# Optimization experiments

Measured on AMD Instinct MI355X. Metric: run time of the kernel, lower is better.

Reference implementation:

```python
import jax, jax.numpy as jnp
import numpy as np

DT = 0.1
TAU_HP = 12.3  # Tm1 high-pass time constant
TAU_LP = 2.3   # Tm1 low-pass time constant

N_NEURONS = 200_000
N_EDGES = 6_400_000
N_TM1 = 25_000
STEPS = 50


def setup_inputs() -> dict:
    key = jax.random.key(0)
    k1, k2, k3, k4 = jax.random.split(key, 4)
    tm1_input = jax.random.normal(k1, (STEPS, N_TM1), dtype=jnp.float32)
    weights = jax.random.normal(k2, (N_EDGES,), dtype=jnp.float32) * 0.1
    tau = jnp.ones((N_NEURONS,), dtype=jnp.float32)      # tau_init = 1.0 per type
    vrest = jnp.zeros((N_NEURONS,), dtype=jnp.float32)   # vrest_init = 0.0 per type
    source_idx = jax.random.randint(k3, (N_EDGES,), 0, N_NEURONS, dtype=jnp.int32)
    target_idx = jax.random.randint(k4, (N_EDGES,), 0, N_NEURONS, dtype=jnp.int32)
    return {
        "tm1_input": tm1_input,
        "weights": weights,
        "tau": tau,
        "vrest": vrest,
        "source_idx": source_idx,
        "target_idx": target_idx,
        "n_tm1": N_TM1,
    }


def reference(tm1_input, weights, tau, vrest, source_idx, target_idx, n_tm1):
    n_neurons = tau.shape[0]

    def step(carry, x):
        v, tm1_f, tm1_v = carry
        # Tm1 temporal filters: high-pass then rectify then low-pass
        hp_out = x - tm1_f                                   # [n_tm1]
        tm1_f_new = tm1_f + DT * (x - tm1_f) / TAU_HP
        rect_out = jax.nn.relu(hp_out)
        # write (old) tm1_v into the Tm1 slice of v before recurrence
        v = v.at[:n_tm1].set(tm1_v)
        tm1_v_new = tm1_v + DT * (rect_out - tm1_v) / TAU_LP
        # gather -> weight -> scatter-add message passing
        r = jax.nn.relu(v)                                   # [n_neurons]
        edge_currents = r[source_idx] * weights              # [n_edges]
        synaptic_input = jax.ops.segment_sum(
            edge_currents, target_idx, num_segments=n_neurons)
        external = jnp.zeros_like(v).at[:n_tm1].set(tm1_v_new)
        dv = (-v + synaptic_input + vrest + external) / tau
        dv = dv.at[:n_tm1].set(0.0)                          # Tm1 driven by its filters
        v = v + DT * dv
        return (v, tm1_f_new, tm1_v_new), None

    v0 = jnp.zeros((tau.shape[0],), dtype=tm1_input.dtype)
    f0 = jnp.zeros((n_tm1,), dtype=tm1_input.dtype)
    tv0 = jnp.zeros((n_tm1,), dtype=tm1_input.dtype)
    (v, _, _), _ = jax.lax.scan(step, (v0, f0, tv0), tm1_input)
    return v[None, :]  # [1, n_neurons], matches torch batch=1
```

## Files before the change

### kernel.cpp

```cpp
#include <hip/hip_runtime.h>
#include <hip/hip_bf16.h>

#define DT 0.1f
#define TAU_HP 12.3f
#define TAU_LP 2.3f
#define SCAN_B 1024

#define BSHIFT 7
#define BMASK 127
#define BMAX 2048
#define CHUNK 32768
#define B4_CAP 6144


__global__ void init_kernel(float* __restrict__ vA,
                            float* __restrict__ tm1_f,
                            int n_neurons, int n_tm1) {
    int i = blockIdx.x * blockDim.x + threadIdx.x;
    if (i < n_neurons) vA[i] = 0.0f;
    if (i < n_tm1) tm1_f[i] = 0.0f;
}

__global__ void bhist_kernel(const int* __restrict__ tgt, int* __restrict__ blkhist,
                             int n_edges, int n_tm1, int nb, int nblk) {
    __shared__ int hist[BMAX];
    int b = blockIdx.x;
    for (int i = threadIdx.x; i < nb; i += blockDim.x) hist[i] = 0;
    __syncthreads();
    int base = b * CHUNK;
    int end = min(base + CHUNK, n_edges);
    for (int k = base + threadIdx.x; k < end; k += blockDim.x) {
        int t = tgt[k];
        if (t >= n_tm1) atomicAdd(&hist[t >> BSHIFT], 1);
    }
    __syncthreads();
    for (int i = threadIdx.x; i < nb; i += blockDim.x)
        blkhist[(size_t)i * nblk + b] = hist[i];
}

__global__ void scan1_kernel(const int* in, int* out, int* bsums, int n) {
    __shared__ int s[SCAN_B];
    int gid = blockIdx.x * SCAN_B + threadIdx.x;
    int x = (gid < n) ? in[gid] : 0;
    s[threadIdx.x] = x;
    __syncthreads();
    for (int off = 1; off < SCAN_B; off <<= 1) {
        int t = (threadIdx.x >= off) ? s[threadIdx.x - off] : 0;
        __syncthreads();
        s[threadIdx.x] += t;
        __syncthreads();
    }
    if (gid < n) out[gid] = s[threadIdx.x] - x;
    if (threadIdx.x == SCAN_B - 1) bsums[blockIdx.x] = s[SCAN_B - 1];
}

__global__ void scan2_kernel(int* bsums, int nb, int* total) {
    __shared__ int s[SCAN_B];
    int x = (threadIdx.x < nb) ? bsums[threadIdx.x] : 0;
    s[threadIdx.x] = x;
    __syncthreads();
    for (int off = 1; off < SCAN_B; off <<= 1) {
        int t = (threadIdx.x >= off) ? s[threadIdx.x - off] : 0;
        __syncthreads();
        s[threadIdx.x] += t;
        __syncthreads();
    }
    if (threadIdx.x == nb - 1) *total = s[threadIdx.x];
    if (threadIdx.x < nb) bsums[threadIdx.x] = s[threadIdx.x] - x;
}

__global__ void scanadd_kernel(int* data, const int* __restrict__ bsums, int n) {
    int gid = blockIdx.x * blockDim.x + threadIdx.x;
    if (gid < n) data[gid] += bsums[gid / SCAN_B];
}

__global__ void bin_kernel(const int* __restrict__ src, const int* __restrict__ tgt,
                           const float* __restrict__ w, const int* __restrict__ scanned,
                           int2* __restrict__ edges, int n_edges, int n_tm1,
                           int nb, int nblk) {
    __shared__ int cur[BMAX];
    int b = blockIdx.x;
    for (int i = threadIdx.x; i < nb; i += blockDim.x)
        cur[i] = scanned[(size_t)i * nblk + b];
    __syncthreads();
    int base = b * CHUNK;
    int end = min(base + CHUNK, n_edges);
    for (int k = base + threadIdx.x; k < end; k += blockDim.x) {
        int t = tgt[k];
        if (t < n_tm1) continue;
        int pos = atomicAdd(&cur[t >> BSHIFT], 1);
        edges[pos] = make_int2(src[k] | ((t & BMASK) << 18), __float_as_int(w[k]));
    }
}

__global__ void finalize_kernel(int2* edges, const int* __restrict__ scanned,
                                int* __restrict__ row_start,
                                const int* __restrict__ total,
                                int n_neurons, int nb, int nblk) {
    __shared__ int2 buf[B4_CAP];
    __shared__ int hist[BMASK + 1], ls[BMASK + 1], cur[BMASK + 1];
    int b = blockIdx.x;
    int n_kept = *total;
    int beg = scanned[(size_t)b * nblk];
    int end = (b == nb - 1) ? n_kept : scanned[(size_t)(b + 1) * nblk];
    int n = min(end - beg, B4_CAP);

    for (int k = threadIdx.x; k < n; k += blockDim.x) buf[k] = edges[beg + k];
    if (threadIdx.x <= BMASK) hist[threadIdx.x] = 0;
    __syncthreads();
    for (int k = threadIdx.x; k < n; k += blockDim.x)
        atomicAdd(&hist[(buf[k].x >> 18) & BMASK], 1);
    __syncthreads();
    if (threadIdx.x <= BMASK) ls[threadIdx.x] = hist[threadIdx.x];
    __syncthreads();
    for (int off = 1; off <= BMASK; off <<= 1) {
        int t = (threadIdx.x <= BMASK && threadIdx.x >= off) ? ls[threadIdx.x - off] : 0;
        __syncthreads();
        if (threadIdx.x <= BMASK) ls[threadIdx.x] += t;
        __syncthreads();
    }
    if (threadIdx.x <= BMASK) {
        int excl = ls[threadIdx.x] - hist[threadIdx.x];
        cur[threadIdx.x] = excl;
        int t = (b << BSHIFT) + threadIdx.x;
        if (t < n_neurons) row_start[t] = beg + excl;
    }
    if (b == nb - 1 && threadIdx.x == 0) row_start[n_neurons] = n_kept;
    __syncthreads();
    for (int k = threadIdx.x; k < n; k += blockDim.x) {
        int2 r = buf[k];
        int pos = atomicAdd(&cur[(r.x >> 18) & BMASK], 1);
        edges[beg + pos] = make_int2(r.x & 0x3FFFF, r.y);
    }
}

__global__ void step_kernel(const int* __restrict__ row_start,
                            const int2* __restrict__ edges,
                            const float* __restrict__ vr,
                            float* __restrict__ vw,
                            float* __restrict__ tm1_f,
                            const float* __restrict__ x,
                            const float* __restrict__ tau,
                            const float* __restrict__ vrest,
                            int n_neurons, int n_tm1, int gbase, int last) {
    int g = blockIdx.x * blockDim.x + threadIdx.x;

    if (g < n_tm1) {
        float cur = vr[g];
        if (last) {
            vw[g] = cur;
        } else {
            float f  = tm1_f[g];
            float xk = x[g];
            float hp = xk - f;
            tm1_f[g] = f + DT * (xk - f) / TAU_HP;
            vw[g] = cur + DT * (fmaxf(hp, 0.0f) - cur) / TAU_LP;
        }
        return;
    }
    if (g < gbase) return;

    int t = g - gbase;
    int row = n_tm1 + (t >> 3);
    if (row >= n_neurons) return;
    int lane = t & 7;

    int s = row_start[row];
    int e = row_start[row + 1];
    float sum = 0.0f;
    for (int p = (s & ~1) + 2 * lane; p < e; p += 16) {
        int4 q = *(const int4*)(edges + p);
        if (p >= s)    sum += fmaxf(vr[q.x], 0.0f) * __int_as_float(q.y);
        if (p + 1 < e) sum += fmaxf(vr[q.z], 0.0f) * __int_as_float(q.w);
    }
    sum += __shfl_xor(sum, 4);
    sum += __shfl_xor(sum, 2);
    sum += __shfl_xor(sum, 1);
    if (lane == 0) {
        float vi = vr[row];
        vw[row] = vi + DT * ((-vi + sum + vrest[row]) / tau[row]);
    }
}

extern "C" void kernel_launch(void* const* d_in, const int* in_sizes, int n_in,
                              void* d_out, int out_size, void* d_ws, size_t ws_size,
                              hipStream_t stream) {
    const float* tm1_input  = (const float*)d_in[0];
    const float* weights    = (const float*)d_in[1];
    const float* tau        = (const float*)d_in[2];
    const float* vrest      = (const float*)d_in[3];
    const int*   source_idx = (const int*)d_in[4];
    const int*   target_idx = (const int*)d_in[5];

    const int n_edges   = in_sizes[1];
    const int n_neurons = in_sizes[2];
    const int n_tm1     = 25000;
    const int steps     = in_sizes[0] / n_tm1;

    const int nb   = (n_neurons + BMASK) >> BSHIFT;
    const int nblk = (n_edges + CHUNK - 1) / CHUNK;
    const int n_scan = nb * nblk;

    size_t off = 0;
    auto alloc = [&](size_t n) { size_t o = off; off += n; return o; };
    int* ws_i = (int*)d_ws;
    float* ws_f = (float*)d_ws;

    int2*  edges     = (int2*)(ws_i + alloc((size_t)(n_edges + 2) * 2));
    float* vA        = ws_f + alloc(n_neurons);
    float* vB        = ws_f + alloc(n_neurons);
    float* tm1_f     = ws_f + alloc(n_tm1);
    int*   row_start = ws_i + alloc(n_neurons + 1);
    int*   blkhist   = ws_i + alloc((size_t)n_scan);
    int*   bsums     = ws_i + alloc(SCAN_B);
    int*   total     = ws_i + alloc(1);
    (void)ws_size;

    float* out = (float*)d_out;

    const int B = 256;
    const int gridN = (n_neurons + B - 1) / B;
    const int nScanBlocks = (n_scan + SCAN_B - 1) / SCAN_B;
    const int gridSA = (n_scan + B - 1) / B;

    const int gbase = (n_tm1 + 63) & ~63;
    const int work  = gbase + (n_neurons - n_tm1) * 8;
    const int gridG = (work + B - 1) / B;

    init_kernel<<<gridN, B, 0, stream>>>(vA, tm1_f, n_neurons, n_tm1);
    bhist_kernel<<<nblk, 1024, 0, stream>>>(target_idx, blkhist, n_edges, n_tm1,
                                            nb, nblk);
    scan1_kernel<<<nScanBlocks, SCAN_B, 0, stream>>>(blkhist, blkhist, bsums, n_scan);
    scan2_kernel<<<1, SCAN_B, 0, stream>>>(bsums, nScanBlocks, total);
    scanadd_kernel<<<gridSA, B, 0, stream>>>(blkhist, bsums, n_scan);
    bin_kernel<<<nblk, 1024, 0, stream>>>(source_idx, target_idx, weights, blkhist,
                                          edges, n_edges, n_tm1, nb, nblk);
    finalize_kernel<<<nb, 1024, 0, stream>>>(edges, blkhist, row_start, total,
                                             n_neurons, nb, nblk);

    for (int k = 0; k < steps; ++k) {
        const float* vr = (k & 1) ? vB : vA;
        float* vw = (k == steps - 1) ? out : ((k & 1) ? vA : vB);
        step_kernel<<<gridG, B, 0, stream>>>(
            row_start, edges, vr, vw, tm1_f,
            tm1_input + (size_t)k * n_tm1,
            tau, vrest, n_neurons, n_tm1, gbase, (k == steps - 1) ? 1 : 0);
    }
}
```

Baseline: 1.876 ms.

## Skip gathers from non-positive neurons using a per-step positivity bitmask

Each step now writes a bitmask marking which neurons ended with positive voltage, built with wave ballots and atomicOr. The next step's edge loop checks this compact bitmask before loading the source voltage, so it skips the scattered gather for neurons whose ReLU output is zero. Three mask buffers rotate so one can be cleared while another is read and a third is written. The cost is an extra bitmask load per edge, atomics per wave, and divergent branches in the gather loop. The benefit depends on how sparse the activity is, and early steps, where most voltages are zero, gain the most.

Measured after the change: 2.180 ms. 1.16x slower.

```diff
diff --git a/kernel.cpp b/kernel.cpp
--- a/kernel.cpp
+++ b/kernel.cpp
@@ -15,10 +15,12 @@
 
 __global__ void init_kernel(float* __restrict__ vA,
                             float* __restrict__ tm1_f,
-                            int n_neurons, int n_tm1) {
+                            unsigned* __restrict__ mask3,
+                            int n_neurons, int n_tm1, int mask3_words) {
     int i = blockIdx.x * blockDim.x + threadIdx.x;
     if (i < n_neurons) vA[i] = 0.0f;
     if (i < n_tm1) tm1_f[i] = 0.0f;
+    if (i < mask3_words) mask3[i] = 0u;
 }
 
 __global__ void bhist_kernel(const int* __restrict__ tgt, int* __restrict__ blkhist,
@@ -142,43 +144,75 @@
                             const float* __restrict__ x,
                             const float* __restrict__ tau,
                             const float* __restrict__ vrest,
+                            const unsigned* __restrict__ maskR,
+                            unsigned* __restrict__ maskW,
+                            unsigned* __restrict__ maskC,
+                            int mask_words,
                             int n_neurons, int n_tm1, int gbase, int last) {
     int g = blockIdx.x * blockDim.x + threadIdx.x;
 
-    if (g < n_tm1) {
-        float cur = vr[g];
-        if (last) {
-            vw[g] = cur;
-        } else {
-            float f  = tm1_f[g];
-            float xk = x[g];
-            float hp = xk - f;
-            tm1_f[g] = f + DT * (xk - f) / TAU_HP;
-            vw[g] = cur + DT * (fmaxf(hp, 0.0f) - cur) / TAU_LP;
+    if (g < gbase) {
+        if (g < mask_words) maskC[g] = 0u;
+        float val = 0.0f;
+        bool wrote = false;
+        if (g < n_tm1) {
+            float cur = vr[g];
+            if (last) {
+                val = cur;
+            } else {
+                float f  = tm1_f[g];
+                float xk = x[g];
+                float hp = xk - f;
+                tm1_f[g] = f + DT * (xk - f) / TAU_HP;
+                val = cur + DT * (fmaxf(hp, 0.0f) - cur) / TAU_LP;
+            }
+            vw[g] = val;
+            wrote = true;
         }
+        unsigned long long bm = __ballot(wrote && (val > 0.0f));
+        int l = threadIdx.x & 63;
+        unsigned lo = (unsigned)(bm & 0xffffffffull);
+        unsigned hi = (unsigned)(bm >> 32);
+        if (l == 0 && lo)  atomicOr(&maskW[g >> 5], lo);
+        if (l == 32 && hi) atomicOr(&maskW[g >> 5], hi);
         return;
     }
-    if (g < gbase) return;
 
     int t = g - gbase;
     int row = n_tm1 + (t >> 3);
-    if (row >= n_neurons) return;
     int lane = t & 7;
-
-    int s = row_start[row];
-    int e = row_start[row + 1];
+    bool active = (row < n_neurons);
     float sum = 0.0f;
-    for (int p = (s & ~1) + 2 * lane; p < e; p += 16) {
-        int4 q = *(const int4*)(edges + p);
-        if (p >= s)    sum += fmaxf(vr[q.x], 0.0f) * __int_as_float(q.y);
-        if (p + 1 < e) sum += fmaxf(vr[q.z], 0.0f) * __int_as_float(q.w);
+    float vnew = 0.0f;
+
+    if (active) {
+        int s = row_start[row];
+        int e = row_start[row + 1];
+        for (int p = (s & ~1) + 2 * lane; p < e; p += 16) {
+            int4 q = *(const int4*)(edges + p);
+            if (p >= s && ((maskR[q.x >> 5] >> (q.x & 31)) & 1u))
+                sum += vr[q.x] * __int_as_float(q.y);
+            if (p + 1 < e && ((maskR[q.z >> 5] >> (q.z & 31)) & 1u))
+                sum += vr[q.z] * __int_as_float(q.w);
+        }
     }
     sum += __shfl_xor(sum, 4);
     sum += __shfl_xor(sum, 2);
     sum += __shfl_xor(sum, 1);
-    if (lane == 0) {
+    if (active && lane == 0) {
         float vi = vr[row];
-        vw[row] = vi + DT * ((-vi + sum + vrest[row]) / tau[row]);
+        vnew = vi + DT * ((-vi + sum + vrest[row]) / tau[row]);
+        vw[row] = vnew;
+    }
+    unsigned long long bm = __ballot(active && lane == 0 && vnew > 0.0f);
+    if ((threadIdx.x & 63) == 0) {
+        unsigned b8 = 0;
+        #pragma unroll
+        for (int i = 0; i < 8; ++i) b8 |= (unsigned)((bm >> (8 * i)) & 1ull) << i;
+        if (b8) {
+            int row0 = n_tm1 + (t >> 3);
+            atomicOr(&maskW[row0 >> 5], b8 << (row0 & 31));
+        }
     }
 }
 
@@ -200,20 +234,22 @@
     const int nb   = (n_neurons + BMASK) >> BSHIFT;
     const int nblk = (n_edges + CHUNK - 1) / CHUNK;
     const int n_scan = nb * nblk;
+    const int mask_words = (n_neurons + 31) >> 5;
 
     size_t off = 0;
     auto alloc = [&](size_t n) { size_t o = off; off += n; return o; };
     int* ws_i = (int*)d_ws;
     float* ws_f = (float*)d_ws;
 
-    int2*  edges     = (int2*)(ws_i + alloc((size_t)(n_edges + 2) * 2));
-    float* vA        = ws_f + alloc(n_neurons);
-    float* vB        = ws_f + alloc(n_neurons);
-    float* tm1_f     = ws_f + alloc(n_tm1);
-    int*   row_start = ws_i + alloc(n_neurons + 1);
-    int*   blkhist   = ws_i + alloc((size_t)n_scan);
-    int*   bsums     = ws_i + alloc(SCAN_B);
-    int*   total     = ws_i + alloc(1);
+    int2*     edges     = (int2*)(ws_i + alloc((size_t)(n_edges + 2) * 2));
+    float*    vA        = ws_f + alloc(n_neurons);
+    float*    vB        = ws_f + alloc(n_neurons);
+    float*    tm1_f     = ws_f + alloc(n_tm1);
+    int*      row_start = ws_i + alloc(n_neurons + 1);
+    unsigned* mask3     = (unsigned*)(ws_i + alloc((size_t)3 * mask_words));
+    int*      blkhist   = ws_i + alloc((size_t)n_scan);
+    int*      bsums     = ws_i + alloc(SCAN_B);
+    int*      total     = ws_i + alloc(1);
     (void)ws_size;
 
     float* out = (float*)d_out;
@@ -227,7 +263,8 @@
     const int work  = gbase + (n_neurons - n_tm1) * 8;
     const int gridG = (work + B - 1) / B;
 
-    init_kernel<<<gridN, B, 0, stream>>>(vA, tm1_f, n_neurons, n_tm1);
+    init_kernel<<<gridN, B, 0, stream>>>(vA, tm1_f, mask3, n_neurons, n_tm1,
+                                         3 * mask_words);
     bhist_kernel<<<nblk, 1024, 0, stream>>>(target_idx, blkhist, n_edges, n_tm1,
                                             nb, nblk);
     scan1_kernel<<<nScanBlocks, SCAN_B, 0, stream>>>(blkhist, blkhist, bsums, n_scan);
@@ -241,9 +278,13 @@
     for (int k = 0; k < steps; ++k) {
         const float* vr = (k & 1) ? vB : vA;
         float* vw = (k == steps - 1) ? out : ((k & 1) ? vA : vB);
+        unsigned* mW = mask3 + (size_t)(k % 3) * mask_words;
+        unsigned* mR = mask3 + (size_t)((k + 2) % 3) * mask_words;
+        unsigned* mC = mask3 + (size_t)((k + 1) % 3) * mask_words;
         step_kernel<<<gridG, B, 0, stream>>>(
             row_start, edges, vr, vw, tm1_f,
             tm1_input + (size_t)k * n_tm1,
-            tau, vrest, n_neurons, n_tm1, gbase, (k == steps - 1) ? 1 : 0);
-    }
-}
+            tau, vrest, mR, mW, mC, mask_words,
+            n_neurons, n_tm1, gbase, (k == steps - 1) ? 1 : 0);
+    }
+}
```

## Tile edges by target-row block and source range, gathering from LDS

Applied to the files above, without the earlier changes.

Replaces the CSR per-row gather with a 2D binning of edges by 512-row target block and 16K-neuron source range. Each step kernel block stages the relu'd source tile in shared memory and accumulates into a per-row LDS accumulator with shared atomics. The aim is to turn random global gathers of v into LDS reads. In exchange the block reloads up to 13 source tiles per step, runs only about 391 blocks, relies on heavy LDS atomic contention, and makes the float summation order nondeterministic.

Measured after the change: 3.552 ms. +89.3%, slower.

```diff
diff --git a/kernel.cpp b/kernel.cpp
--- a/kernel.cpp
+++ b/kernel.cpp
@@ -5,12 +5,13 @@
 #define TAU_HP 12.3f
 #define TAU_LP 2.3f
 #define SCAN_B 1024
-
-#define BSHIFT 7
-#define BMASK 127
-#define BMAX 2048
 #define CHUNK 32768
-#define B4_CAP 6144
+
+#define RB 512
+#define RBBITS 9
+#define SR 16384
+#define SRBITS 14
+#define BKMAX 5120
 
 
 __global__ void init_kernel(float* __restrict__ vA,
@@ -21,20 +22,23 @@
     if (i < n_tm1) tm1_f[i] = 0.0f;
 }
 
-__global__ void bhist_kernel(const int* __restrict__ tgt, int* __restrict__ blkhist,
-                             int n_edges, int n_tm1, int nb, int nblk) {
-    __shared__ int hist[BMAX];
+__global__ void bhist_kernel(const int* __restrict__ src,
+                             const int* __restrict__ tgt,
+                             int* __restrict__ blkhist,
+                             int n_edges, int n_tm1, int nbkt, int NR, int nblk) {
+    __shared__ int hist[BKMAX];
     int b = blockIdx.x;
-    for (int i = threadIdx.x; i < nb; i += blockDim.x) hist[i] = 0;
+    for (int i = threadIdx.x; i < nbkt; i += blockDim.x) hist[i] = 0;
     __syncthreads();
     int base = b * CHUNK;
     int end = min(base + CHUNK, n_edges);
     for (int k = base + threadIdx.x; k < end; k += blockDim.x) {
         int t = tgt[k];
-        if (t >= n_tm1) atomicAdd(&hist[t >> BSHIFT], 1);
-    }
-    __syncthreads();
-    for (int i = threadIdx.x; i < nb; i += blockDim.x)
+        if (t >= n_tm1)
+            atomicAdd(&hist[(t >> RBBITS) * NR + (src[k] >> SRBITS)], 1);
+    }
+    __syncthreads();
+    for (int i = threadIdx.x; i < nbkt; i += blockDim.x)
         blkhist[(size_t)i * nblk + b] = hist[i];
 }
 
@@ -77,10 +81,10 @@
 __global__ void bin_kernel(const int* __restrict__ src, const int* __restrict__ tgt,
                            const float* __restrict__ w, const int* __restrict__ scanned,
                            int2* __restrict__ edges, int n_edges, int n_tm1,
-                           int nb, int nblk) {
-    __shared__ int cur[BMAX];
+                           int nbkt, int NR, int nblk) {
+    __shared__ int cur[BKMAX];
     int b = blockIdx.x;
-    for (int i = threadIdx.x; i < nb; i += blockDim.x)
+    for (int i = threadIdx.x; i < nbkt; i += blockDim.x)
         cur[i] = scanned[(size_t)i * nblk + b];
     __syncthreads();
     int base = b * CHUNK;
@@ -88,97 +92,91 @@
     for (int k = base + threadIdx.x; k < end; k += blockDim.x) {
         int t = tgt[k];
         if (t < n_tm1) continue;
-        int pos = atomicAdd(&cur[t >> BSHIFT], 1);
-        edges[pos] = make_int2(src[k] | ((t & BMASK) << 18), __float_as_int(w[k]));
-    }
-}
-
-__global__ void finalize_kernel(int2* edges, const int* __restrict__ scanned,
-                                int* __restrict__ row_start,
-                                const int* __restrict__ total,
-                                int n_neurons, int nb, int nblk) {
-    __shared__ int2 buf[B4_CAP];
-    __shared__ int hist[BMASK + 1], ls[BMASK + 1], cur[BMASK + 1];
+        int s = src[k];
+        int key = (t >> RBBITS) * NR + (s >> SRBITS);
+        int pos = atomicAdd(&cur[key], 1);
+        edges[pos] = make_int2((s & (SR - 1)) | ((t & (RB - 1)) << SRBITS),
+                               __float_as_int(w[k]));
+    }
+}
+
+__global__ void mkseg_kernel(const int* __restrict__ scanned, int* __restrict__ seg,
+                             const int* __restrict__ total, int nbkt, int nblk) {
+    int i = blockIdx.x * blockDim.x + threadIdx.x;
+    if (i < nbkt) seg[i] = scanned[(size_t)i * nblk];
+    if (i == nbkt) seg[nbkt] = *total;
+}
+
+__global__ __launch_bounds__(1024)
+void step2_kernel(const int* __restrict__ seg,
+                  const int2* __restrict__ edges,
+                  const float* __restrict__ vr,
+                  float* __restrict__ vw,
+                  float* __restrict__ tm1_f,
+                  const float* __restrict__ x,
+                  const float* __restrict__ tau,
+                  const float* __restrict__ vrest,
+                  int n_neurons, int n_tm1, int NR, int last) {
+    __shared__ float tile[SR];
+    __shared__ float acc[RB];
+    int tid = threadIdx.x;
     int b = blockIdx.x;
-    int n_kept = *total;
-    int beg = scanned[(size_t)b * nblk];
-    int end = (b == nb - 1) ? n_kept : scanned[(size_t)(b + 1) * nblk];
-    int n = min(end - beg, B4_CAP);
-
-    for (int k = threadIdx.x; k < n; k += blockDim.x) buf[k] = edges[beg + k];
-    if (threadIdx.x <= BMASK) hist[threadIdx.x] = 0;
-    __syncthreads();
-    for (int k = threadIdx.x; k < n; k += blockDim.x)
-        atomicAdd(&hist[(buf[k].x >> 18) & BMASK], 1);
-    __syncthreads();
-    if (threadIdx.x <= BMASK) ls[threadIdx.x] = hist[threadIdx.x];
-    __syncthreads();
-    for (int off = 1; off <= BMASK; off <<= 1) {
-        int t = (threadIdx.x <= BMASK && threadIdx.x >= off) ? ls[threadIdx.x - off] : 0;
-        __syncthreads();
-        if (threadIdx.x <= BMASK) ls[threadIdx.x] += t;
-        __syncthreads();
-    }
-    if (threadIdx.x <= BMASK) {
-        int excl = ls[threadIdx.x] - hist[threadIdx.x];
-        cur[threadIdx.x] = excl;
-        int t = (b << BSHIFT) + threadIdx.x;
-        if (t < n_neurons) row_start[t] = beg + excl;
-    }
-    if (b == nb - 1 && threadIdx.x == 0) row_start[n_neurons] = n_kept;
-    __syncthreads();
-    for (int k = threadIdx.x; k < n; k += blockDim.x) {
-        int2 r = buf[k];
-        int pos = atomicAdd(&cur[(r.x >> 18) & BMASK], 1);
-        edges[beg + pos] = make_int2(r.x & 0x3FFFF, r.y);
-    }
-}
-
-__global__ void step_kernel(const int* __restrict__ row_start,
-                            const int2* __restrict__ edges,
-                            const float* __restrict__ vr,
-                            float* __restrict__ vw,
-                            float* __restrict__ tm1_f,
-                            const float* __restrict__ x,
-                            const float* __restrict__ tau,
-                            const float* __restrict__ vrest,
-                            int n_neurons, int n_tm1, int gbase, int last) {
-    int g = blockIdx.x * blockDim.x + threadIdx.x;
-
-    if (g < n_tm1) {
-        float cur = vr[g];
-        if (last) {
-            vw[g] = cur;
-        } else {
-            float f  = tm1_f[g];
-            float xk = x[g];
-            float hp = xk - f;
-            tm1_f[g] = f + DT * (xk - f) / TAU_HP;
-            vw[g] = cur + DT * (fmaxf(hp, 0.0f) - cur) / TAU_LP;
+    int rowbase = b << RBBITS;
+    if (tid < RB) acc[tid] = 0.0f;
+
+    int segbase = b * NR;
+    int e_first = seg[segbase];
+    int e_last  = seg[segbase + NR];
+
+    if (e_last > e_first) {
+        for (int r = 0; r < NR; ++r) {
+            int e0 = seg[segbase + r], e1 = seg[segbase + r + 1];
+            if (e1 == e0) continue;
+            int sbase = r << SRBITS;
+            if (sbase + SR <= n_neurons) {
+                const float4* v4 = (const float4*)(vr + sbase);
+                float4* t4 = (float4*)tile;
+                for (int i = tid; i < SR / 4; i += 1024) {
+                    float4 v = v4[i];
+                    v.x = fmaxf(v.x, 0.0f); v.y = fmaxf(v.y, 0.0f);
+                    v.z = fmaxf(v.z, 0.0f); v.w = fmaxf(v.w, 0.0f);
+                    t4[i] = v;
+                }
+            } else {
+                for (int i = tid; i < SR; i += 1024) {
+                    int g = sbase + i;
+                    tile[i] = (g < n_neurons) ? fmaxf(vr[g], 0.0f) : 0.0f;
+                }
+            }
+            __syncthreads();
+            for (int e = e0 + tid; e < e1; e += 1024) {
+                int2 rec = edges[e];
+                atomicAdd(&acc[rec.x >> SRBITS],
+                          tile[rec.x & (SR - 1)] * __int_as_float(rec.y));
+            }
+            __syncthreads();
         }
-        return;
-    }
-    if (g < gbase) return;
-
-    int t = g - gbase;
-    int row = n_tm1 + (t >> 3);
-    if (row >= n_neurons) return;
-    int lane = t & 7;
-
-    int s = row_start[row];
-    int e = row_start[row + 1];
-    float sum = 0.0f;
-    for (int p = (s & ~1) + 2 * lane; p < e; p += 16) {
-        int4 q = *(const int4*)(edges + p);
-        if (p >= s)    sum += fmaxf(vr[q.x], 0.0f) * __int_as_float(q.y);
-        if (p + 1 < e) sum += fmaxf(vr[q.z], 0.0f) * __int_as_float(q.w);
-    }
-    sum += __shfl_xor(sum, 4);
-    sum += __shfl_xor(sum, 2);
-    sum += __shfl_xor(sum, 1);
-    if (lane == 0) {
-        float vi = vr[row];
-        vw[row] = vi + DT * ((-vi + sum + vrest[row]) / tau[row]);
+    }
+
+    if (tid < RB) {
+        int row = rowbase + tid;
+        if (row < n_neurons) {
+            if (row < n_tm1) {
+                float cur = vr[row];
+                if (last) {
+                    vw[row] = cur;
+                } else {
+                    float f  = tm1_f[row];
+                    float xk = x[row];
+                    float hp = xk - f;
+                    tm1_f[row] = f + DT * (xk - f) / TAU_HP;
+                    vw[row] = cur + DT * (fmaxf(hp, 0.0f) - cur) / TAU_LP;
+                }
+            } else {
+                float vi = vr[row];
+                vw[row] = vi + DT * ((-vi + acc[tid] + vrest[row]) / tau[row]);
+            }
+        }
     }
 }
 
@@ -197,23 +195,25 @@
     const int n_tm1     = 25000;
     const int steps     = in_sizes[0] / n_tm1;
 
-    const int nb   = (n_neurons + BMASK) >> BSHIFT;
-    const int nblk = (n_edges + CHUNK - 1) / CHUNK;
-    const int n_scan = nb * nblk;
+    const int NR     = (n_neurons + SR - 1) / SR;
+    const int nbRows = (n_neurons + RB - 1) / RB;
+    const int nbkt   = nbRows * NR;
+    const int nblk   = (n_edges + CHUNK - 1) / CHUNK;
+    const int n_scan = nbkt * nblk;
 
     size_t off = 0;
     auto alloc = [&](size_t n) { size_t o = off; off += n; return o; };
     int* ws_i = (int*)d_ws;
     float* ws_f = (float*)d_ws;
 
-    int2*  edges     = (int2*)(ws_i + alloc((size_t)(n_edges + 2) * 2));
-    float* vA        = ws_f + alloc(n_neurons);
-    float* vB        = ws_f + alloc(n_neurons);
-    float* tm1_f     = ws_f + alloc(n_tm1);
-    int*   row_start = ws_i + alloc(n_neurons + 1);
-    int*   blkhist   = ws_i + alloc((size_t)n_scan);
-    int*   bsums     = ws_i + alloc(SCAN_B);
-    int*   total     = ws_i + alloc(1);
+    int2*  edges   = (int2*)(ws_i + alloc((size_t)(n_edges + 2) * 2));
+    float* vA      = ws_f + alloc(n_neurons);
+    float* vB      = ws_f + alloc(n_neurons);
+    float* tm1_f   = ws_f + alloc(n_tm1);
+    int*   seg     = ws_i + alloc(nbkt + 1);
+    int*   blkhist = ws_i + alloc((size_t)n_scan);
+    int*   bsums   = ws_i + alloc(SCAN_B);
+    int*   total   = ws_i + alloc(1);
     (void)ws_size;
 
     float* out = (float*)d_out;
@@ -222,28 +222,24 @@
     const int gridN = (n_neurons + B - 1) / B;
     const int nScanBlocks = (n_scan + SCAN_B - 1) / SCAN_B;
     const int gridSA = (n_scan + B - 1) / B;
-
-    const int gbase = (n_tm1 + 63) & ~63;
-    const int work  = gbase + (n_neurons - n_tm1) * 8;
-    const int gridG = (work + B - 1) / B;
+    const int gridSeg = (nbkt + 1 + B - 1) / B;
 
     init_kernel<<<gridN, B, 0, stream>>>(vA, tm1_f, n_neurons, n_tm1);
-    bhist_kernel<<<nblk, 1024, 0, stream>>>(target_idx, blkhist, n_edges, n_tm1,
-                                            nb, nblk);
+    bhist_kernel<<<nblk, 1024, 0, stream>>>(source_idx, target_idx, blkhist,
+                                            n_edges, n_tm1, nbkt, NR, nblk);
     scan1_kernel<<<nScanBlocks, SCAN_B, 0, stream>>>(blkhist, blkhist, bsums, n_scan);
     scan2_kernel<<<1, SCAN_B, 0, stream>>>(bsums, nScanBlocks, total);
     scanadd_kernel<<<gridSA, B, 0, stream>>>(blkhist, bsums, n_scan);
     bin_kernel<<<nblk, 1024, 0, stream>>>(source_idx, target_idx, weights, blkhist,
-                                          edges, n_edges, n_tm1, nb, nblk);
-    finalize_kernel<<<nb, 1024, 0, stream>>>(edges, blkhist, row_start, total,
-                                             n_neurons, nb, nblk);
+                                          edges, n_edges, n_tm1, nbkt, NR, nblk);
+    mkseg_kernel<<<gridSeg, B, 0, stream>>>(blkhist, seg, total, nbkt, nblk);
 
     for (int k = 0; k < steps; ++k) {
         const float* vr = (k & 1) ? vB : vA;
         float* vw = (k == steps - 1) ? out : ((k & 1) ? vA : vB);
-        step_kernel<<<gridG, B, 0, stream>>>(
-            row_start, edges, vr, vw, tm1_f,
+        step2_kernel<<<nbRows, 1024, 0, stream>>>(
+            seg, edges, vr, vw, tm1_f,
             tm1_input + (size_t)k * n_tm1,
-            tau, vrest, n_neurons, n_tm1, gbase, (k == steps - 1) ? 1 : 0);
-    }
-}
+            tau, vrest, n_neurons, n_tm1, NR, (k == steps - 1) ? 1 : 0);
+    }
+}
```
